# Kernel optimization log

Hardware: AMD Instinct MI355X
Metric: run time of the kernel (lower is better)

The kernel has to match this reference:

```python
import jax, jax.numpy as jnp
import numpy as np

MIN_RES, MAX_RES, NUM_LOD, BAND_WIDTH = 16, 512, 8, 19
CODEBOOK_SIZE = 2 ** BAND_WIDTH  # 524288
_b = np.exp((np.log(MAX_RES) - np.log(MIN_RES)) / (NUM_LOD - 1))
LODS = [int(1 + np.floor(MIN_RES * _b ** l)) for l in range(NUM_LOD)]
SIZES = [min(CODEBOOK_SIZE, r ** 3) for r in LODS]
PRIMES = (1, 2654435761, 805459861)  # Instant-NGP spatial hash primes
N_PTS = 2_000_000

# corner offsets of the unit cube, [8,3]
_OFFS = np.array([[(i >> 2) & 1, (i >> 1) & 1, i & 1] for i in range(8)], dtype=np.int32)


def _hash_interp(p01, table, res, size):
    """Hashed trilinear interpolation for one LOD. p01:[N,3] in [0,1], table:[size]."""
    x = p01 * (res - 1)                                   # [N,3]
    c0 = jnp.clip(jnp.floor(x), 0, res - 2).astype(jnp.int32)
    frac = x - c0.astype(jnp.float32)                     # [N,3]
    offs = jnp.asarray(_OFFS)                             # [8,3]
    corners = (c0[:, None, :] + offs[None]).astype(jnp.uint32)  # [N,8,3]
    h = (corners[..., 0] * jnp.uint32(PRIMES[0])
         ^ corners[..., 1] * jnp.uint32(PRIMES[1])
         ^ corners[..., 2] * jnp.uint32(PRIMES[2]))
    idx = (h % jnp.uint32(size)).astype(jnp.int32)        # [N,8]
    feats = table[idx]                                    # [N,8] gather
    offf = offs.astype(jnp.float32)
    # trilinear weights: prod_d (frac if offset else 1-frac)
    w = jnp.prod(frac[:, None, :] * offf + (1.0 - frac[:, None, :]) * (1.0 - offf), axis=-1)
    return jnp.sum(w * feats, axis=-1)                    # [N]


def setup_inputs() -> dict:
    key = jax.random.key(0)
    k1, k2 = jax.random.split(key)
    pts = jax.random.uniform(k1, (N_PTS, 3), jnp.float32) * 2.0 - 1.0  # [-1,1]^3
    codebook = jax.random.normal(k2, (NUM_LOD, CODEBOOK_SIZE, 1), jnp.float32) * 0.01
    return {"pts": pts, "codebook": codebook}


def reference(pts, codebook):
    p01 = pts / 2.0 + 0.5                                  # normalize to [0,1]
    out = jnp.zeros(pts.shape[0], jnp.float32)
    for i, res in enumerate(LODS):                         # small static loop over LODs
        table = codebook[i, : SIZES[i], 0]                 # static slice -> actual table size
        out = out + _hash_interp(p01, table, res, SIZES[i])
    return out[:, None]                                    # [N, feat_dim=1]
```

## Files before the change

### kernel.cpp

```cpp
#include <hip/hip_runtime.h>
#include <math.h>


static constexpr unsigned CB_STRIDE = 524288u;
static constexpr int S0 = 4913;
static constexpr int S1 = 19683;
static constexpr int WO2 = 0;
static constexpr int WO3 = 85184;
static constexpr int WO4 = 443104;
static constexpr int WO5 = 967392;
static constexpr int WO6 = 1491680;
static constexpr int WO7 = 2015968;
static constexpr size_t WS_NEED_BYTES = 2540256u * 2u;

__device__ __forceinline__ unsigned short f32_to_bf16_rne(float f) {
    unsigned u = __float_as_uint(f);
    u = (u + 0x7FFFu + ((u >> 16) & 1u)) >> 16;
    return (unsigned short)u;
}
__device__ __forceinline__ float bf16_to_f32(unsigned short s) {
    return __uint_as_float(((unsigned)s) << 16);
}

struct I8 { unsigned a0, a1, a2, a3, a4, a5, a6, a7; };
struct R8 { unsigned short v0, v1, v2, v3, v4, v5, v6, v7; };
struct W3 { float x, y, z; };

template <unsigned SIZE, bool POW2>
__device__ __forceinline__ I8 idx8(float p01x, float p01y, float p01z, int res, W3& fr)
{
    const float rm1 = (float)(res - 1);
    float xx = p01x * rm1, yy = p01y * rm1, zz = p01z * rm1;
    const float cmax = (float)(res - 2);
    float fx = fminf(fmaxf(floorf(xx), 0.0f), cmax);
    float fy = fminf(fmaxf(floorf(yy), 0.0f), cmax);
    float fz = fminf(fmaxf(floorf(zz), 0.0f), cmax);
    fr.x = xx - fx; fr.y = yy - fy; fr.z = zz - fz;
    const unsigned ix = (unsigned)(int)fx;
    const unsigned iy = (unsigned)(int)fy;
    const unsigned iz = (unsigned)(int)fz;

    const unsigned hx0 = ix;
    const unsigned hx1 = ix + 1u;
    const unsigned hy0 = iy * 2654435761u;
    const unsigned hy1 = hy0 + 2654435761u;
    const unsigned hz0 = iz * 805459861u;
    const unsigned hz1 = hz0 + 805459861u;

    unsigned v0 = hx0 ^ hy0 ^ hz0;
    unsigned v1 = hx0 ^ hy0 ^ hz1;
    unsigned v2 = hx0 ^ hy1 ^ hz0;
    unsigned v3 = hx0 ^ hy1 ^ hz1;
    unsigned v4 = hx1 ^ hy0 ^ hz0;
    unsigned v5 = hx1 ^ hy0 ^ hz1;
    unsigned v6 = hx1 ^ hy1 ^ hz0;
    unsigned v7 = hx1 ^ hy1 ^ hz1;

    if (POW2) {
        const unsigned m = SIZE - 1u;
        v0 &= m; v1 &= m; v2 &= m; v3 &= m; v4 &= m; v5 &= m; v6 &= m; v7 &= m;
    } else {
        v0 %= SIZE; v1 %= SIZE; v2 %= SIZE; v3 %= SIZE;
        v4 %= SIZE; v5 %= SIZE; v6 %= SIZE; v7 %= SIZE;
    }
    I8 o; o.a0 = v0; o.a1 = v1; o.a2 = v2; o.a3 = v3;
          o.a4 = v4; o.a5 = v5; o.a6 = v6; o.a7 = v7;
    return o;
}

__device__ __forceinline__ R8 gather8(const unsigned short* __restrict__ t, I8 o)
{
    R8 r;
    r.v0 = t[o.a0]; r.v1 = t[o.a1]; r.v2 = t[o.a2]; r.v3 = t[o.a3];
    r.v4 = t[o.a4]; r.v5 = t[o.a5]; r.v6 = t[o.a6]; r.v7 = t[o.a7];
    return r;
}

__device__ __forceinline__ float acc8(R8 r, W3 f)
{
    const float wx1 = f.x, wx0 = 1.0f - f.x;
    const float wy1 = f.y, wy0 = 1.0f - f.y;
    const float wz1 = f.z, wz0 = 1.0f - f.z;
    const float w00 = wy0 * wz0, w01 = wy0 * wz1;
    const float w10 = wy1 * wz0, w11 = wy1 * wz1;
    const float sx0 = bf16_to_f32(r.v0) * w00 + bf16_to_f32(r.v1) * w01
                    + bf16_to_f32(r.v2) * w10 + bf16_to_f32(r.v3) * w11;
    const float sx1 = bf16_to_f32(r.v4) * w00 + bf16_to_f32(r.v5) * w01
                    + bf16_to_f32(r.v6) * w10 + bf16_to_f32(r.v7) * w11;
    return wx0 * sx0 + wx1 * sx1;
}

__global__ __launch_bounds__(1024)
void HashGrid_convert_kernel(const float* __restrict__ codebook,
                             unsigned short* __restrict__ ws)
{
    const int lod = blockIdx.y;
    const int sizes[6] = {85184, 357911, 524288, 524288, 524288, 524288};
    const int offs[6]  = {WO2, WO3, WO4, WO5, WO6, WO7};
    const int idx = blockIdx.x * 1024 + threadIdx.x;
    if (idx < sizes[lod])
        ws[offs[lod] + idx] = f32_to_bf16_rne(codebook[(unsigned)(lod + 2) * CB_STRIDE + idx]);
}

__global__ __launch_bounds__(1024, 8)
void HashGrid_88278757802387_kernel(const float* __restrict__ pts,
                                    const float* __restrict__ codebook,
                                    const unsigned short* __restrict__ ws,
                                    float* __restrict__ out,
                                    int n, int res7)
{
    __shared__ unsigned short sm[S0 + S1];
    for (int j = threadIdx.x; j < S0 + S1; j += 1024)
        sm[j] = f32_to_bf16_rne(j < S0 ? codebook[j] : codebook[CB_STRIDE + (j - S0)]);
    __syncthreads();

    const int i = blockIdx.x * 1024 + threadIdx.x;
    if (i >= n) return;

    const float p01x = pts[3 * i + 0] * 0.5f + 0.5f;
    const float p01y = pts[3 * i + 1] * 0.5f + 0.5f;
    const float p01z = pts[3 * i + 2] * 0.5f + 0.5f;

    W3 fA, fB, fC, fD, fE, fF, fL0, fL1;
    I8 oA = idx8<85184u,  false>(p01x, p01y, p01z, 44, fA);
    I8 oB = idx8<357911u, false>(p01x, p01y, p01z, 71, fB);
    R8 rA = gather8(ws + WO2, oA);
    R8 rB = gather8(ws + WO3, oB);

    I8 oC = idx8<524288u, true>(p01x, p01y, p01z, 116, fC);
    R8 rC = gather8(ws + WO4, oC);

    I8 oL0 = idx8<4913u,  false>(p01x, p01y, p01z, 17, fL0);
    I8 oL1 = idx8<19683u, false>(p01x, p01y, p01z, 27, fL1);
    R8 rL0 = gather8(sm, oL0);
    R8 rL1 = gather8(sm + S0, oL1);
    float acc = acc8(rL0, fL0) + acc8(rL1, fL1);

    I8 oD = idx8<524288u, true>(p01x, p01y, p01z, 191, fD);
    R8 rD = gather8(ws + WO5, oD);
    acc += acc8(rA, fA);

    I8 oE = idx8<524288u, true>(p01x, p01y, p01z, 313, fE);
    R8 rE = gather8(ws + WO6, oE);
    acc += acc8(rB, fB);

    I8 oF = idx8<524288u, true>(p01x, p01y, p01z, res7, fF);
    R8 rF = gather8(ws + WO7, oF);
    acc += acc8(rC, fC);

    acc += acc8(rD, fD);
    acc += acc8(rE, fE);
    acc += acc8(rF, fF);

    out[i] = acc;
}

__global__ __launch_bounds__(1024, 4)
void HashGrid_fallback_kernel(const float* __restrict__ pts,
                              const float* __restrict__ codebook,
                              float* __restrict__ out,
                              int n, int res7)
{
    const int i = blockIdx.x * 1024 + threadIdx.x;
    if (i >= n) return;
    const float p01x = pts[3 * i + 0] * 0.5f + 0.5f;
    const float p01y = pts[3 * i + 1] * 0.5f + 0.5f;
    const float p01z = pts[3 * i + 2] * 0.5f + 0.5f;
    float acc = 0.0f;
    const int      reslist[8]  = {17, 27, 44, 71, 116, 191, 313, res7};
    const unsigned sizelist[8] = {4913u, 19683u, 85184u, 357911u, 524288u, 524288u, 524288u, 524288u};
    for (int l = 0; l < 8; ++l) {
        const int res = reslist[l];
        const unsigned size = sizelist[l];
        const float rm1 = (float)(res - 1);
        float xx = p01x * rm1, yy = p01y * rm1, zz = p01z * rm1;
        float fx = fminf(fmaxf(floorf(xx), 0.0f), (float)(res - 2));
        float fy = fminf(fmaxf(floorf(yy), 0.0f), (float)(res - 2));
        float fz = fminf(fmaxf(floorf(zz), 0.0f), (float)(res - 2));
        const float frx = xx - fx, fry = yy - fy, frz = zz - fz;
        const unsigned ix = (unsigned)(int)fx, iy = (unsigned)(int)fy, iz = (unsigned)(int)fz;
        const unsigned hy0 = iy * 2654435761u, hy1 = hy0 + 2654435761u;
        const unsigned hz0 = iz * 805459861u,  hz1 = hz0 + 805459861u;
        const unsigned o0 = (ix ^ hy0 ^ hz0) % size,      o1 = (ix ^ hy0 ^ hz1) % size;
        const unsigned o2 = (ix ^ hy1 ^ hz0) % size,      o3 = (ix ^ hy1 ^ hz1) % size;
        const unsigned o4 = ((ix+1u) ^ hy0 ^ hz0) % size, o5 = ((ix+1u) ^ hy0 ^ hz1) % size;
        const unsigned o6 = ((ix+1u) ^ hy1 ^ hz0) % size, o7 = ((ix+1u) ^ hy1 ^ hz1) % size;
        const float* tab = codebook + (unsigned)l * CB_STRIDE;
        const float wx1 = frx, wx0 = 1.0f - frx;
        const float wy1 = fry, wy0 = 1.0f - fry;
        const float wz1 = frz, wz0 = 1.0f - frz;
        const float w00 = wy0*wz0, w01 = wy0*wz1, w10 = wy1*wz0, w11 = wy1*wz1;
        acc += wx0 * (tab[o0]*w00 + tab[o1]*w01 + tab[o2]*w10 + tab[o3]*w11)
             + wx1 * (tab[o4]*w00 + tab[o5]*w01 + tab[o6]*w10 + tab[o7]*w11);
    }
    out[i] = acc;
}

extern "C" void kernel_launch(void* const* d_in, const int* in_sizes, int n_in,
                              void* d_out, int out_size, void* d_ws, size_t ws_size,
                              hipStream_t stream)
{
    const float* pts      = (const float*)d_in[0];
    const float* codebook = (const float*)d_in[1];
    float* out            = (float*)d_out;
    const int n = in_sizes[0] / 3;

    const double b = exp((log(512.0) - log(16.0)) / 7.0);
    const int res7 = (int)(1.0 + floor(16.0 * pow(b, 7.0)));

    const bool use_ws = (d_ws != nullptr) && (ws_size >= WS_NEED_BYTES);
    const int blocks = (n + 1023) / 1024;

    if (use_ws) {
        unsigned short* ws = (unsigned short*)d_ws;
        hipLaunchKernelGGL(HashGrid_convert_kernel, dim3(512, 6), dim3(1024),
                           0, stream, codebook, ws);
        hipLaunchKernelGGL(HashGrid_88278757802387_kernel, dim3(blocks), dim3(1024),
                           0, stream, pts, codebook, ws, out, n, res7);
    } else {
        hipLaunchKernelGGL(HashGrid_fallback_kernel, dim3(blocks), dim3(1024),
                           0, stream, pts, codebook, out, n, res7);
    }
}
```

Measured before the change: 407.8 us.

## Merge x-adjacent hash corners into paired 32-bit loads for power-of-two LODs

For the four LODs with a power-of-two table size, the x-corner hash differs only in bit 0 when ix is even, so both x corners are fetched with one aligned 32-bit load. A second 16-bit gather runs only when ix is odd. This can cut the gather count for those LODs by up to half. The change also reorders work so the pow2 LODs are computed eagerly rather than interleaved, which may reduce how many loads are in flight at once and adds divergent branches.

```diff
diff --git a/kernel.cpp b/kernel.cpp
--- a/kernel.cpp
+++ b/kernel.cpp
@@ -90,6 +90,71 @@
     return wx0 * sx0 + wx1 * sx1;
 }
 
+__device__ __forceinline__ void unpack2(unsigned pair, unsigned sel, bool oddx,
+                                        unsigned short oval, float& v0, float& v1)
+{
+    const unsigned short lo = (unsigned short)(pair & 0xffffu);
+    const unsigned short hi = (unsigned short)(pair >> 16);
+    const unsigned short e0 = sel ? hi : lo;
+    const unsigned short eo = sel ? lo : hi;
+    v0 = bf16_to_f32(e0);
+    v1 = bf16_to_f32(oddx ? oval : eo);
+}
+
+__device__ __forceinline__ float lod_pow2_merged(float p01x, float p01y, float p01z,
+                                                 int res,
+                                                 const unsigned short* __restrict__ t)
+{
+    const float rm1 = (float)(res - 1);
+    float xx = p01x * rm1, yy = p01y * rm1, zz = p01z * rm1;
+    const float cmax = (float)(res - 2);
+    float fx = fminf(fmaxf(floorf(xx), 0.0f), cmax);
+    float fy = fminf(fmaxf(floorf(yy), 0.0f), cmax);
+    float fz = fminf(fmaxf(floorf(zz), 0.0f), cmax);
+    const float frx = xx - fx, fry = yy - fy, frz = zz - fz;
+    const unsigned ix = (unsigned)(int)fx;
+    const unsigned iy = (unsigned)(int)fy;
+    const unsigned iz = (unsigned)(int)fz;
+
+    const unsigned hy0 = iy * 2654435761u, hy1 = hy0 + 2654435761u;
+    const unsigned hz0 = iz * 805459861u,  hz1 = hz0 + 805459861u;
+    const unsigned m = 524287u;
+
+    const unsigned I00 = (ix ^ hy0 ^ hz0) & m;
+    const unsigned I01 = (ix ^ hy0 ^ hz1) & m;
+    const unsigned I10 = (ix ^ hy1 ^ hz0) & m;
+    const unsigned I11 = (ix ^ hy1 ^ hz1) & m;
+
+    const unsigned p00 = *reinterpret_cast<const unsigned*>(t + (I00 & ~1u));
+    const unsigned p01 = *reinterpret_cast<const unsigned*>(t + (I01 & ~1u));
+    const unsigned p10 = *reinterpret_cast<const unsigned*>(t + (I10 & ~1u));
+    const unsigned p11 = *reinterpret_cast<const unsigned*>(t + (I11 & ~1u));
+
+    const unsigned hx1 = ix + 1u;
+    const unsigned J00 = (hx1 ^ hy0 ^ hz0) & m;
+    const unsigned J01 = (hx1 ^ hy0 ^ hz1) & m;
+    const unsigned J10 = (hx1 ^ hy1 ^ hz0) & m;
+    const unsigned J11 = (hx1 ^ hy1 ^ hz1) & m;
+    unsigned short o00 = 0, o01 = 0, o10 = 0, o11 = 0;
+    const bool oddx = (ix & 1u) != 0u;
+    if (oddx) { o00 = t[J00]; o01 = t[J01]; o10 = t[J10]; o11 = t[J11]; }
+
+    float v000, v100, v001, v101, v010, v110, v011, v111;
+    unpack2(p00, I00 & 1u, oddx, o00, v000, v100);
+    unpack2(p01, I01 & 1u, oddx, o01, v001, v101);
+    unpack2(p10, I10 & 1u, oddx, o10, v010, v110);
+    unpack2(p11, I11 & 1u, oddx, o11, v011, v111);
+
+    const float wx1 = frx, wx0 = 1.0f - frx;
+    const float wy1 = fry, wy0 = 1.0f - fry;
+    const float wz1 = frz, wz0 = 1.0f - frz;
+    const float w00 = wy0 * wz0, w01 = wy0 * wz1;
+    const float w10 = wy1 * wz0, w11 = wy1 * wz1;
+    const float sx0 = v000 * w00 + v001 * w01 + v010 * w10 + v011 * w11;
+    const float sx1 = v100 * w00 + v101 * w01 + v110 * w10 + v111 * w11;
+    return wx0 * sx0 + wx1 * sx1;
+}
+
 __global__ __launch_bounds__(1024)
 void HashGrid_convert_kernel(const float* __restrict__ codebook,
                              unsigned short* __restrict__ ws)
@@ -121,36 +186,24 @@
     const float p01y = pts[3 * i + 1] * 0.5f + 0.5f;
     const float p01z = pts[3 * i + 2] * 0.5f + 0.5f;
 
-    W3 fA, fB, fC, fD, fE, fF, fL0, fL1;
+    W3 fA, fB, fL0, fL1;
     I8 oA = idx8<85184u,  false>(p01x, p01y, p01z, 44, fA);
     I8 oB = idx8<357911u, false>(p01x, p01y, p01z, 71, fB);
     R8 rA = gather8(ws + WO2, oA);
     R8 rB = gather8(ws + WO3, oB);
 
-    I8 oC = idx8<524288u, true>(p01x, p01y, p01z, 116, fC);
-    R8 rC = gather8(ws + WO4, oC);
+    float acc = lod_pow2_merged(p01x, p01y, p01z, 116,  ws + WO4);
+    acc      += lod_pow2_merged(p01x, p01y, p01z, 191,  ws + WO5);
+    acc      += lod_pow2_merged(p01x, p01y, p01z, 313,  ws + WO6);
+    acc      += lod_pow2_merged(p01x, p01y, p01z, res7, ws + WO7);
 
     I8 oL0 = idx8<4913u,  false>(p01x, p01y, p01z, 17, fL0);
     I8 oL1 = idx8<19683u, false>(p01x, p01y, p01z, 27, fL1);
     R8 rL0 = gather8(sm, oL0);
     R8 rL1 = gather8(sm + S0, oL1);
-    float acc = acc8(rL0, fL0) + acc8(rL1, fL1);
-
-    I8 oD = idx8<524288u, true>(p01x, p01y, p01z, 191, fD);
-    R8 rD = gather8(ws + WO5, oD);
-    acc += acc8(rA, fA);
-
-    I8 oE = idx8<524288u, true>(p01x, p01y, p01z, 313, fE);
-    R8 rE = gather8(ws + WO6, oE);
-    acc += acc8(rB, fB);
-
-    I8 oF = idx8<524288u, true>(p01x, p01y, p01z, res7, fF);
-    R8 rF = gather8(ws + WO7, oF);
-    acc += acc8(rC, fC);
-
-    acc += acc8(rD, fD);
-    acc += acc8(rE, fE);
-    acc += acc8(rF, fF);
+    acc += acc8(rL0, fL0) + acc8(rL1, fL1);
+
+    acc += acc8(rA, fA) + acc8(rB, fB);
 
     out[i] = acc;
 }
```

New measurement: 458.4 us. +12.4%, slower.
